# Kernel optimization log

Measured on AMD Instinct MI355X. Metric: run time of the kernel, lower is better.

The kernel has to match this reference:

```python
import jax, jax.numpy as jnp
import numpy as np

POOL, D_MODEL, D_FF, M_DIM = 512, 1024, 4096, 64
B, S, K = 2, 2048, 8


def setup_inputs() -> dict:
    key = jax.random.key(0)
    ks = jax.random.split(key, 8)
    x = jax.random.normal(ks[0], (B, S, D_MODEL), dtype=jnp.float32)
    selected_indices = jax.random.randint(ks[1], (B, S, K), 0, POOL, dtype=jnp.int32)
    pattern_weights = jax.random.normal(ks[2], (B, S, K), dtype=jnp.float32)
    base_patterns = 0.02 * jax.random.normal(ks[3], (POOL, D_FF), dtype=jnp.float32)
    # nn.Linear(d_model, pool_size*mod_dim): weight [P*M, d_model], xavier-uniform
    lim_cm = float(np.sqrt(6.0 / (D_MODEL + POOL * M_DIM)))
    cm_w = jax.random.uniform(ks[4], (POOL * M_DIM, D_MODEL), jnp.float32, -lim_cm, lim_cm)
    cm_b = jnp.zeros((POOL * M_DIM,), jnp.float32)
    adj_proj = 0.01 * jax.random.normal(ks[5], (M_DIM, D_FF), dtype=jnp.float32)
    lim_w2 = float(np.sqrt(6.0 / (D_FF + D_MODEL)))
    w2_w = jax.random.uniform(ks[6], (D_MODEL, D_FF), jnp.float32, -lim_w2, lim_w2)
    w2_b = jnp.zeros((D_MODEL,), jnp.float32)
    return {"x": x, "selected_indices": selected_indices, "pattern_weights": pattern_weights,
            "base_patterns": base_patterns, "cm_w": cm_w, "cm_b": cm_b,
            "adj_proj": adj_proj, "w2_w": w2_w, "w2_b": w2_b}


def reference(x, selected_indices, pattern_weights, base_patterns, cm_w, cm_b, adj_proj, w2_w, w2_b):
    b, s, k = selected_indices.shape
    # gather base firing patterns for selected neurons: [b,s,k,d_ff]
    bp = base_patterns[selected_indices]
    # dense context modulation then gather (matches original module): [b,s,P,M]
    mod = (jnp.einsum('bsd,nd->bsn', x, cm_w) + cm_b).reshape(b, s, POOL, M_DIM)
    sel_mod = jnp.take_along_axis(mod, selected_indices[..., None], axis=2)  # [b,s,k,M]
    adjustments = jnp.einsum('bskm,mf->bskf', sel_mod, adj_proj)
    adjusted = bp + adjustments  # [b,s,k,d_ff]
    w = jax.nn.softmax(pattern_weights, axis=-1)
    combined = jnp.einsum('bsk,bskf->bsf', w, adjusted)  # [b,s,d_ff]
    activated = jax.nn.gelu(combined, approximate=False)  # torch default gelu = exact erf
    return jnp.einsum('bsf,df->bsd', activated, w2_w) + w2_b
```

## Files before the change

### kernel.cpp

```cpp
#include <hip/hip_runtime.h>
#include <math.h>

#define T_    4096
#define K_    8
#define POOL_ 512
#define DM_   1024
#define DFF_  4096
#define MD_   64
#define KC_   576
#define NSPLIT 4

typedef __bf16 bf16x8 __attribute__((ext_vector_type(8)));
typedef __bf16 bf16x4 __attribute__((ext_vector_type(4)));
typedef float  f32x4  __attribute__((ext_vector_type(4)));

typedef __attribute__((address_space(1))) const void g_void;
typedef __attribute__((address_space(3))) void s_void;

__device__ __forceinline__ void async_ld16(const void* g, void* s) {
    __builtin_amdgcn_global_load_lds((g_void*)g, (s_void*)s, 16, 0, 0);
}
__device__ __forceinline__ float gelu_exact(float g) {
    return 0.5f * g * (1.f + erff(g * 0.70710678118654752f));
}

__global__ __launch_bounds__(256) void k_hist(const int* __restrict__ sel,
                                              int* __restrict__ counts) {
    int i = blockIdx.x * 256 + threadIdx.x;
    if (i < T_ * K_) atomicAdd(&counts[sel[i]], 1);
}

__global__ __launch_bounds__(512) void k_scan(const int* __restrict__ counts,
                                              int* __restrict__ offsets,
                                              int* __restrict__ cursor) {
    __shared__ int s[512];
    const int t = threadIdx.x;
    const int c = counts[t];
    s[t] = c;
    __syncthreads();
    for (int d = 1; d < 512; d <<= 1) {
        int v = (t >= d) ? s[t - d] : 0;
        __syncthreads();
        s[t] += v;
        __syncthreads();
    }
    offsets[t] = s[t] - c;
    cursor[t]  = s[t] - c;
    if (t == 511) offsets[512] = s[511];
}

__global__ __launch_bounds__(256) void k_scatter(const int* __restrict__ sel,
                                                 int* __restrict__ cursor,
                                                 int* __restrict__ bucket) {
    int i = blockIdx.x * 256 + threadIdx.x;
    if (i < T_ * K_) {
        int p = sel[i];
        int pos = atomicAdd(&cursor[p], 1);
        bucket[pos] = i;
    }
}

__global__ __launch_bounds__(256, 8) void k_selmod(
    const float* __restrict__ x, const float* __restrict__ cm_w,
    const int* __restrict__ bucket, const int* __restrict__ offsets,
    float* __restrict__ Yp)
{
    const int p     = blockIdx.x;
    const int slice = blockIdx.y;
    const int tid   = threadIdx.x;
    __shared__ __align__(16) __bf16 Xl[64][72];
    __shared__ __align__(16) __bf16 Wl[64][72];

    const int off = offsets[p];
    const int n   = min(offsets[p + 1] - off, 1024);
    if (n == 0) return;

    const int wave = tid >> 6, lane = tid & 63, quad = lane >> 4, l15 = lane & 15;
    const int srow = tid & 63;
    const int c0   = (tid >> 6) * 16;
    const int k0   = slice * (DM_ / NSPLIT);

    const float* wrow = cm_w + (long)(p * 64 + srow) * DM_ + k0;
    float* Yo = Yp + (long)slice * ((long)T_ * K_ * MD_);

    for (int base = 0; base < n; base += 64) {
        f32x4 acc[4] = {};
        int li = base + srow; if (li >= n) li = n - 1;
        const float* xrow = x + (long)(bucket[off + li] >> 3) * DM_ + k0;

        for (int kc = 0; kc < DM_ / NSPLIT; kc += 64) {
            const float4* xs = (const float4*)(xrow + kc + c0);
            const float4* ws = (const float4*)(wrow + kc + c0);
            #pragma unroll
            for (int u = 0; u < 4; ++u) {
                float4 xv = xs[u], wv = ws[u];
                bf16x4 xb, wb;
                xb[0]=(__bf16)xv.x; xb[1]=(__bf16)xv.y; xb[2]=(__bf16)xv.z; xb[3]=(__bf16)xv.w;
                wb[0]=(__bf16)wv.x; wb[1]=(__bf16)wv.y; wb[2]=(__bf16)wv.z; wb[3]=(__bf16)wv.w;
                *(bf16x4*)&Xl[srow][c0 + u * 4] = xb;
                *(bf16x4*)&Wl[srow][c0 + u * 4] = wb;
            }
            __syncthreads();
            #pragma unroll
            for (int ks = 0; ks < 2; ++ks) {
                const int ko = ks * 32 + quad * 8;
                bf16x8 bfr = *(const bf16x8*)&Wl[wave * 16 + l15][ko];
                #pragma unroll
                for (int i = 0; i < 4; ++i) {
                    bf16x8 afr = *(const bf16x8*)&Xl[i * 16 + l15][ko];
                    acc[i] = __builtin_amdgcn_mfma_f32_16x16x32_bf16(afr, bfr, acc[i], 0, 0, 0);
                }
            }
            __syncthreads();
        }
        const int mcol = wave * 16 + l15;
        #pragma unroll
        for (int i = 0; i < 4; ++i) {
            #pragma unroll
            for (int r = 0; r < 4; ++r) {
                int prow = base + i * 16 + quad * 4 + r;
                if (prow < n)
                    Yo[(long)bucket[off + prow] * MD_ + mcol] = acc[i][r];
            }
        }
    }
}

__global__ __launch_bounds__(256) void k_wdense(
    const float* __restrict__ Yp, const int* __restrict__ sel,
    const float* __restrict__ pw, const float* __restrict__ cm_b,
    __bf16* __restrict__ Wd)
{
    const int tid = threadIdx.x;
    const int tt = tid >> 6, m = tid & 63;
    const int t = blockIdx.x * 4 + tt;
    __shared__ float w_s[4][8];
    __shared__ int   sidx[4][8];
    __shared__ __align__(16) __bf16 row[4][KC_];

    if (m < 8) {
        w_s[tt][m]  = pw[t * 8 + m];
        sidx[tt][m] = sel[t * 8 + m];
    }
    __syncthreads();
    if (m == 0) {
        float mx = w_s[tt][0];
        #pragma unroll
        for (int k = 1; k < 8; ++k) mx = fmaxf(mx, w_s[tt][k]);
        float sum = 0.f;
        #pragma unroll
        for (int k = 0; k < 8; ++k) { float e = expf(w_s[tt][k] - mx); w_s[tt][k] = e; sum += e; }
        float inv = 1.f / sum;
        #pragma unroll
        for (int k = 0; k < 8; ++k) w_s[tt][k] *= inv;
    }
    __syncthreads();
    *(uint4*)&row[tt][m * 8] = make_uint4(0, 0, 0, 0);
    {
        const long YN = (long)T_ * K_ * MD_;
        float a = 0.f;
        #pragma unroll
        for (int k = 0; k < 8; ++k) {
            const long base = ((long)t * 8 + k) * MD_ + m;
            float y = cm_b[sidx[tt][k] * 64 + m];
            #pragma unroll
            for (int s = 0; s < NSPLIT; ++s) y += Yp[s * YN + base];
            a += w_s[tt][k] * y;
        }
        row[tt][512 + m] = (__bf16)a;
    }
    __syncthreads();
    if (m == 0) {
        #pragma unroll
        for (int k = 0; k < 8; ++k) {
            int c = sidx[tt][k];
            row[tt][c] = (__bf16)((float)row[tt][c] + w_s[tt][k]);
        }
    }
    __syncthreads();
    const uint4* src = (const uint4*)&row[0][0];
    uint4* dst = (uint4*)(Wd + (long)blockIdx.x * 4 * KC_);
    for (int e = tid; e < 4 * KC_ * 2 / 16; e += 256) dst[e] = src[e];
}

__global__ __launch_bounds__(256) void k_buildP(
    const float* __restrict__ bp, const float* __restrict__ adj,
    __bf16* __restrict__ P)
{
    __shared__ __bf16 tile[64][72];
    const int tid = threadIdx.x;
    const int bx = blockIdx.x, f0 = blockIdx.y * 64;
    const float* src = (bx < 8) ? (bp + (long)bx * 64 * DFF_) : adj;
    for (int e = tid; e < 4096; e += 256) {
        int f = e & 63, c = e >> 6;
        tile[c][f] = (__bf16)src[(long)c * DFF_ + f0 + f];
    }
    __syncthreads();
    const int c0 = bx * 64;
    for (int e = tid; e < 4096; e += 256) {
        int c = e & 63, f = e >> 6;
        P[(long)(f0 + f) * KC_ + c0 + c] = tile[c][f];
    }
}

__global__ __launch_bounds__(256) void k_cvt(const float* __restrict__ src,
                                             __bf16* __restrict__ dst, int n16) {
    int i = blockIdx.x * 256 + threadIdx.x;
    if (i >= n16) return;
    const float4* s = (const float4*)src + (long)i * 4;
    float4 a = s[0], b = s[1], c = s[2], d = s[3];
    bf16x8 o0, o1;
    o0[0]=(__bf16)a.x; o0[1]=(__bf16)a.y; o0[2]=(__bf16)a.z; o0[3]=(__bf16)a.w;
    o0[4]=(__bf16)b.x; o0[5]=(__bf16)b.y; o0[6]=(__bf16)b.z; o0[7]=(__bf16)b.w;
    o1[0]=(__bf16)c.x; o1[1]=(__bf16)c.y; o1[2]=(__bf16)c.z; o1[3]=(__bf16)c.w;
    o1[4]=(__bf16)d.x; o1[5]=(__bf16)d.y; o1[6]=(__bf16)d.z; o1[7]=(__bf16)d.w;
    bf16x8* dp = (bf16x8*)dst + (long)i * 2;
    dp[0] = o0; dp[1] = o1;
}

__global__ __launch_bounds__(256) void k_actgemm(
    const __bf16* __restrict__ A, const __bf16* __restrict__ Bw,
    __bf16* __restrict__ act)
{
    __shared__ __align__(16) __bf16 sA[128 * 32];
    __shared__ __align__(16) __bf16 sB[128 * 32];
    const int tid  = threadIdx.x;
    const int tm   = blockIdx.y * 128, tn = blockIdx.x * 128;
    const int wave = tid >> 6, lane = tid & 63, quad = lane >> 4, l15 = lane & 15;
    const int wm   = (wave >> 1) * 64, wn = (wave & 1) * 64;

    f32x4 acc[4][4] = {};

    const int e    = tid * 8;
    const int srow = e >> 5;
    const int scol = e & 31;
    const __bf16* agp0 = A  + ((long)(tm + srow)      * KC_ + scol);
    const __bf16* agp1 = A  + ((long)(tm + 64 + srow) * KC_ + scol);
    const __bf16* bgp0 = Bw + ((long)(tn + srow)      * KC_ + scol);
    const __bf16* bgp1 = Bw + ((long)(tn + 64 + srow) * KC_ + scol);
    void* sa0 = (void*)(sA + e);
    void* sa1 = (void*)(sA + 2048 + e);
    void* sb0 = (void*)(sB + e);
    void* sb1 = (void*)(sB + 2048 + e);

    for (int kk = 0; kk < KC_; kk += 32) {
        async_ld16(agp0 + kk, sa0);
        async_ld16(agp1 + kk, sa1);
        async_ld16(bgp0 + kk, sb0);
        async_ld16(bgp1 + kk, sb1);
        __syncthreads();
        bf16x8 af[4], bf[4];
        #pragma unroll
        for (int i = 0; i < 4; ++i)
            af[i] = *(const bf16x8*)(sA + (wm + i * 16 + l15) * 32 + quad * 8);
        #pragma unroll
        for (int j = 0; j < 4; ++j)
            bf[j] = *(const bf16x8*)(sB + (wn + j * 16 + l15) * 32 + quad * 8);
        #pragma unroll
        for (int i = 0; i < 4; ++i)
            #pragma unroll
            for (int j = 0; j < 4; ++j)
                acc[i][j] = __builtin_amdgcn_mfma_f32_16x16x32_bf16(af[i], bf[j], acc[i][j], 0, 0, 0);
        __syncthreads();
    }

    #pragma unroll
    for (int j = 0; j < 4; ++j) {
        const int col = tn + wn + j * 16 + l15;
        #pragma unroll
        for (int i = 0; i < 4; ++i) {
            const int row = tm + wm + i * 16 + quad * 4;
            #pragma unroll
            for (int r = 0; r < 4; ++r)
                act[(long)(row + r) * DFF_ + col] = (__bf16)gelu_exact(acc[i][j][r]);
        }
    }
}

__global__ __launch_bounds__(256) void k_outgemm(
    const __bf16* __restrict__ A, const __bf16* __restrict__ Bw,
    const float* __restrict__ bias, float* __restrict__ out)
{
    __shared__ __align__(16) __bf16 sA[128 * 128];
    __shared__ __align__(16) __bf16 sB[128 * 128];
    const int tid  = threadIdx.x;
    const int tm   = blockIdx.y * 128, tn = blockIdx.x * 128;
    const int wave = tid >> 6, lane = tid & 63, quad = lane >> 4, l15 = lane & 15;
    const int wm   = (wave >> 1) * 64, wn = (wave & 1) * 64;

    f32x4 acc[4][4] = {};

    const int e  = tid * 8;
    const int r0 = e >> 5;
    const int cc = e & 31;

    for (int kk = 0; kk < DFF_; kk += 128) {
        #pragma unroll
        for (int s = 0; s < 4; ++s) {
            #pragma unroll
            for (int q = 0; q < 2; ++q) {
                async_ld16(A  + (long)(tm + q * 64 + r0) * DFF_ + kk + s * 32 + cc,
                           (void*)(sA + s * 4096 + q * 2048 + e));
                async_ld16(Bw + (long)(tn + q * 64 + r0) * DFF_ + kk + s * 32 + cc,
                           (void*)(sB + s * 4096 + q * 2048 + e));
            }
        }
        __syncthreads();
        #pragma unroll
        for (int s = 0; s < 4; ++s) {
            bf16x8 af[4], bf[4];
            #pragma unroll
            for (int i = 0; i < 4; ++i)
                af[i] = *(const bf16x8*)(sA + s * 4096 + (wm + i * 16 + l15) * 32 + quad * 8);
            #pragma unroll
            for (int j = 0; j < 4; ++j)
                bf[j] = *(const bf16x8*)(sB + s * 4096 + (wn + j * 16 + l15) * 32 + quad * 8);
            #pragma unroll
            for (int i = 0; i < 4; ++i)
                #pragma unroll
                for (int j = 0; j < 4; ++j)
                    acc[i][j] = __builtin_amdgcn_mfma_f32_16x16x32_bf16(af[i], bf[j], acc[i][j], 0, 0, 0);
        }
        __syncthreads();
    }

    #pragma unroll
    for (int j = 0; j < 4; ++j) {
        const int col = tn + wn + j * 16 + l15;
        const float bj = bias[col];
        #pragma unroll
        for (int i = 0; i < 4; ++i) {
            const int row = tm + wm + i * 16 + quad * 4;
            #pragma unroll
            for (int r = 0; r < 4; ++r)
                out[(long)(row + r) * 1024 + col] = acc[i][j][r] + bj;
        }
    }
}

extern "C" void kernel_launch(void* const* d_in, const int* in_sizes, int n_in,
                              void* d_out, int out_size, void* d_ws, size_t ws_size,
                              hipStream_t stream) {
    const float* x    = (const float*)d_in[0];
    const int*   sel  = (const int*)  d_in[1];
    const float* pw   = (const float*)d_in[2];
    const float* bp   = (const float*)d_in[3];
    const float* cm_w = (const float*)d_in[4];
    const float* cm_b = (const float*)d_in[5];
    const float* adj  = (const float*)d_in[6];
    const float* w2   = (const float*)d_in[7];
    const float* w2b  = (const float*)d_in[8];
    float* out = (float*)d_out;

    char* ws = (char*)d_ws;
    float*  Yp   = (float*)ws;
    __bf16* act  = (__bf16*)ws;
    __bf16* P    = (__bf16*)(ws + (size_t)32 * 1024 * 1024);
    __bf16* w2bf = (__bf16*)(ws + (size_t)37 * 1024 * 1024);
    char*  bins  = ws + (size_t)45 * 1024 * 1024;
    int* bucket  = (int*)bins;
    int* counts  = (int*)(bins + 131072);
    int* cursor  = (int*)(bins + 133120);
    int* offsets = (int*)(bins + 135168);

    __bf16* Wd = (__bf16*)d_out;

    hipMemsetAsync(counts, 0, 4096, stream);
    k_hist   <<<128, 256, 0, stream>>>(sel, counts);
    k_scan   <<<1,   512, 0, stream>>>(counts, offsets, cursor);
    k_scatter<<<128, 256, 0, stream>>>(sel, cursor, bucket);
    k_selmod <<<dim3(POOL_, NSPLIT), 256, 0, stream>>>(x, cm_w, bucket, offsets, Yp);
    k_wdense <<<T_ / 4, 256, 0, stream>>>(Yp, sel, pw, cm_b, Wd);
    k_buildP <<<dim3(9, 64), 256, 0, stream>>>(bp, adj, P);
    k_cvt    <<<1024, 256, 0, stream>>>(w2, w2bf, DM_ * DFF_ / 16);
    k_actgemm<<<dim3(DFF_ / 128, T_ / 128), 256, 0, stream>>>(Wd, P, act);
    k_outgemm<<<dim3(DM_ / 128, T_ / 128), 256, 0, stream>>>(act, w2bf, w2b, out);
}
```

Baseline: 441.2 us.

## Coalesce selmod loads and write partial projections in bucket order via rank map

```diff
diff --git a/kernel.cpp b/kernel.cpp
--- a/kernel.cpp
+++ b/kernel.cpp
@@ -9,6 +9,7 @@
 #define MD_   64
 #define KC_   576
 #define NSPLIT 4
+#define NCAP  256
 
 typedef __bf16 bf16x8 __attribute__((ext_vector_type(8)));
 typedef __bf16 bf16x4 __attribute__((ext_vector_type(4)));
@@ -22,6 +23,11 @@
 }
 __device__ __forceinline__ float gelu_exact(float g) {
     return 0.5f * g * (1.f + erff(g * 0.70710678118654752f));
+}
+__device__ __forceinline__ bf16x4 cvt4(float4 v) {
+    bf16x4 o;
+    o[0] = (__bf16)v.x; o[1] = (__bf16)v.y; o[2] = (__bf16)v.z; o[3] = (__bf16)v.w;
+    return o;
 }
 
 __global__ __launch_bounds__(256) void k_hist(const int* __restrict__ sel,
@@ -51,12 +57,14 @@
 
 __global__ __launch_bounds__(256) void k_scatter(const int* __restrict__ sel,
                                                  int* __restrict__ cursor,
-                                                 int* __restrict__ bucket) {
+                                                 int* __restrict__ bucket,
+                                                 int* __restrict__ rank) {
     int i = blockIdx.x * 256 + threadIdx.x;
     if (i < T_ * K_) {
         int p = sel[i];
         int pos = atomicAdd(&cursor[p], 1);
         bucket[pos] = i;
+        rank[i] = pos;
     }
 }
 
@@ -68,37 +76,45 @@
     const int p     = blockIdx.x;
     const int slice = blockIdx.y;
     const int tid   = threadIdx.x;
+    __shared__ int list[NCAP];
     __shared__ __align__(16) __bf16 Xl[64][72];
     __shared__ __align__(16) __bf16 Wl[64][72];
 
     const int off = offsets[p];
-    const int n   = min(offsets[p + 1] - off, 1024);
+    const int n   = min(offsets[p + 1] - off, NCAP);
     if (n == 0) return;
+    for (int i = tid; i < n; i += 256) list[i] = bucket[off + i] >> 3;
+    __syncthreads();
 
     const int wave = tid >> 6, lane = tid & 63, quad = lane >> 4, l15 = lane & 15;
-    const int srow = tid & 63;
-    const int c0   = (tid >> 6) * 16;
+    const int srow = tid >> 3;
+    const int part = tid & 7;
     const int k0   = slice * (DM_ / NSPLIT);
 
-    const float* wrow = cm_w + (long)(p * 64 + srow) * DM_ + k0;
+    const float* w0 = cm_w + (long)(p * 64 + srow)      * DM_ + k0;
+    const float* w1 = cm_w + (long)(p * 64 + srow + 32) * DM_ + k0;
     float* Yo = Yp + (long)slice * ((long)T_ * K_ * MD_);
 
     for (int base = 0; base < n; base += 64) {
         f32x4 acc[4] = {};
-        int li = base + srow; if (li >= n) li = n - 1;
-        const float* xrow = x + (long)(bucket[off + li] >> 3) * DM_ + k0;
+        int li0 = base + srow;      if (li0 >= n) li0 = n - 1;
+        int li1 = base + srow + 32; if (li1 >= n) li1 = n - 1;
+        const float* x0 = x + (long)list[li0] * DM_ + k0;
+        const float* x1 = x + (long)list[li1] * DM_ + k0;
 
         for (int kc = 0; kc < DM_ / NSPLIT; kc += 64) {
-            const float4* xs = (const float4*)(xrow + kc + c0);
-            const float4* ws = (const float4*)(wrow + kc + c0);
-            #pragma unroll
-            for (int u = 0; u < 4; ++u) {
-                float4 xv = xs[u], wv = ws[u];
-                bf16x4 xb, wb;
-                xb[0]=(__bf16)xv.x; xb[1]=(__bf16)xv.y; xb[2]=(__bf16)xv.z; xb[3]=(__bf16)xv.w;
-                wb[0]=(__bf16)wv.x; wb[1]=(__bf16)wv.y; wb[2]=(__bf16)wv.z; wb[3]=(__bf16)wv.w;
-                *(bf16x4*)&Xl[srow][c0 + u * 4] = xb;
-                *(bf16x4*)&Wl[srow][c0 + u * 4] = wb;
+            #pragma unroll
+            for (int u = 0; u < 2; ++u) {
+                const int c = kc + u * 32 + part * 4;
+                float4 a0 = *(const float4*)(x0 + c);
+                float4 a1 = *(const float4*)(x1 + c);
+                float4 b0 = *(const float4*)(w0 + c);
+                float4 b1 = *(const float4*)(w1 + c);
+                const int lc = u * 32 + part * 4;
+                *(bf16x4*)&Xl[srow     ][lc] = cvt4(a0);
+                *(bf16x4*)&Xl[srow + 32][lc] = cvt4(a1);
+                *(bf16x4*)&Wl[srow     ][lc] = cvt4(b0);
+                *(bf16x4*)&Wl[srow + 32][lc] = cvt4(b1);
             }
             __syncthreads();
             #pragma unroll
@@ -120,7 +136,7 @@
             for (int r = 0; r < 4; ++r) {
                 int prow = base + i * 16 + quad * 4 + r;
                 if (prow < n)
-                    Yo[(long)bucket[off + prow] * MD_ + mcol] = acc[i][r];
+                    Yo[(long)(off + prow) * MD_ + mcol] = acc[i][r];
             }
         }
     }
@@ -128,19 +144,21 @@
 
 __global__ __launch_bounds__(256) void k_wdense(
     const float* __restrict__ Yp, const int* __restrict__ sel,
-    const float* __restrict__ pw, const float* __restrict__ cm_b,
-    __bf16* __restrict__ Wd)
+    const int* __restrict__ rank, const float* __restrict__ pw,
+    const float* __restrict__ cm_b, __bf16* __restrict__ Wd)
 {
     const int tid = threadIdx.x;
     const int tt = tid >> 6, m = tid & 63;
     const int t = blockIdx.x * 4 + tt;
     __shared__ float w_s[4][8];
     __shared__ int   sidx[4][8];
+    __shared__ int   rnk[4][8];
     __shared__ __align__(16) __bf16 row[4][KC_];
 
     if (m < 8) {
         w_s[tt][m]  = pw[t * 8 + m];
         sidx[tt][m] = sel[t * 8 + m];
+        rnk[tt][m]  = rank[t * 8 + m];
     }
     __syncthreads();
     if (m == 0) {
@@ -161,7 +179,7 @@
         float a = 0.f;
         #pragma unroll
         for (int k = 0; k < 8; ++k) {
-            const long base = ((long)t * 8 + k) * MD_ + m;
+            const long base = (long)rnk[tt][k] * MD_ + m;
             float y = cm_b[sidx[tt][k] * 64 + m];
             #pragma unroll
             for (int s = 0; s < NSPLIT; ++s) y += Yp[s * YN + base];
@@ -359,18 +377,19 @@
     __bf16* w2bf = (__bf16*)(ws + (size_t)37 * 1024 * 1024);
     char*  bins  = ws + (size_t)45 * 1024 * 1024;
     int* bucket  = (int*)bins;
-    int* counts  = (int*)(bins + 131072);
-    int* cursor  = (int*)(bins + 133120);
-    int* offsets = (int*)(bins + 135168);
+    int* rank    = (int*)(bins + 131072);
+    int* counts  = (int*)(bins + 262144);
+    int* cursor  = (int*)(bins + 264192);
+    int* offsets = (int*)(bins + 266240);
 
     __bf16* Wd = (__bf16*)d_out;
 
     hipMemsetAsync(counts, 0, 4096, stream);
     k_hist   <<<128, 256, 0, stream>>>(sel, counts);
     k_scan   <<<1,   512, 0, stream>>>(counts, offsets, cursor);
-    k_scatter<<<128, 256, 0, stream>>>(sel, cursor, bucket);
+    k_scatter<<<128, 256, 0, stream>>>(sel, cursor, bucket, rank);
     k_selmod <<<dim3(POOL_, NSPLIT), 256, 0, stream>>>(x, cm_w, bucket, offsets, Yp);
-    k_wdense <<<T_ / 4, 256, 0, stream>>>(Yp, sel, pw, cm_b, Wd);
+    k_wdense <<<T_ / 4, 256, 0, stream>>>(Yp, sel, rank, pw, cm_b, Wd);
     k_buildP <<<dim3(9, 64), 256, 0, stream>>>(bp, adj, P);
     k_cvt    <<<1024, 256, 0, stream>>>(w2, w2bf, DM_ * DFF_ / 16);
     k_actgemm<<<dim3(DFF_ / 128, T_ / 128), 256, 0, stream>>>(Wd, P, act);
```

Result: faster. 417.5 us (-5.4%).
